# Kernel tuning notes

Hardware: AMD Instinct MI355X
Metric: run time of the kernel (lower is better)

Reference implementation:

```python
import jax, jax.numpy as jnp
import numpy as np

N_NODES = 50000
N_EDGES = 800000
D_IN, D_HID, D_OUT = 16, 64, 16
N_BLOCKS = 4


def setup_inputs() -> dict:
    key = jax.random.key(0)
    ks = jax.random.split(key, 12)
    s = 0.05  # small init scale to keep sum-aggregation over 4 blocks stable
    return {
        "x": jax.random.normal(ks[0], (N_NODES, D_IN), jnp.float32),
        "lframes": jax.random.normal(ks[1], (N_NODES, 4, 4), jnp.float32),
        "edge_index": jax.random.randint(ks[2], (2, N_EDGES), 0, N_NODES, jnp.int64),
        "lin_in_w": jax.random.normal(ks[3], (D_IN, D_HID), jnp.float32) * s,
        "lin_in_b": jnp.zeros((D_HID,), jnp.float32),
        # per-block mlp1: Linear(2D->D), ReLU, Linear(D->D), ReLU, Linear(D->D)
        "w0": jax.random.normal(ks[4], (N_BLOCKS, 2 * D_HID, D_HID), jnp.float32) * s,
        "b0": jnp.zeros((N_BLOCKS, D_HID), jnp.float32),
        "w1": jax.random.normal(ks[5], (N_BLOCKS, D_HID, D_HID), jnp.float32) * s,
        "b1": jnp.zeros((N_BLOCKS, D_HID), jnp.float32),
        "w2": jax.random.normal(ks[6], (N_BLOCKS, D_HID, D_HID), jnp.float32) * s,
        "b2": jnp.zeros((N_BLOCKS, D_HID), jnp.float32),
        "lin_out_w": jax.random.normal(ks[7], (D_HID, D_OUT), jnp.float32) * s,
        "lin_out_b": jnp.zeros((D_OUT,), jnp.float32),
    }


def reference(x, lframes, edge_index, lin_in_w, lin_in_b,
              w0, b0, w1, b1, w2, b2, lin_out_w, lin_out_b):
    src = edge_index[0]  # x_j (source / neighbor)
    dst = edge_index[1]  # x_i (target / aggregation node)
    h = x @ lin_in_w + lin_in_b  # [N, D]
    for k in range(N_BLOCKS):
        # message: cat((x_j, x_i)) -> mlp1 ; mlp2 is Identity (num_layers_mlp2=0)
        m = jnp.concatenate((h[src], h[dst]), axis=-1)  # [E, 2D]
        m = jax.nn.relu(m @ w0[k] + b0[k])
        m = jax.nn.relu(m @ w1[k] + b1[k])
        m = m @ w2[k] + b2[k]  # [E, D]
        # aggregate: scatter-add at target node
        h = jax.ops.segment_sum(m, dst, num_segments=N_NODES)
    return h @ lin_out_w + lin_out_b  # [N, D_OUT]
```

## Files before the change

### kernel.cpp

```cpp
#include <hip/hip_runtime.h>
#include <hip/hip_bf16.h>

#define N_NODES 50000
#define N_EDGES 800000
#define D_IN    16
#define D_HID   64
#define D_OUT   16
#define NCHUNK  ((N_NODES + 255) / 256)
#define TMAX    100352
#define GE8     ((N_EDGES / 8 + 255) / 256)
#define GH      ((N_NODES * D_HID + 255) / 256)
#define SCAP    48
#define NB      98
#define BCAP    12288

typedef __hip_bfloat16 bf16;
typedef _Float16 f16;
typedef _Float16 f16x8 __attribute__((ext_vector_type(8)));
typedef _Float16 f16x4 __attribute__((ext_vector_type(4)));
typedef float    f32x4 __attribute__((ext_vector_type(4)));
typedef _Float16 f16x8a __attribute__((ext_vector_type(8), may_alias));
typedef _Float16 f16x4a __attribute__((ext_vector_type(4), may_alias));
typedef unsigned short u16x8a __attribute__((ext_vector_type(8), may_alias));
typedef float    f32x4a __attribute__((ext_vector_type(4), may_alias));

__device__ __forceinline__ float b2f(bf16 v) { return __bfloat162float(v); }
__device__ __forceinline__ float bfb(unsigned short u) {
    union { unsigned u; float f; } z; z.u = (unsigned)u << 16; return z.f;
}
__device__ __forceinline__ int clampn(int v) {
    return v < 0 ? 0 : (v >= N_NODES ? N_NODES - 1 : v);
}
__device__ __forceinline__ float rdf(const void* p, long i, int isbf) {
    return isbf ? b2f(((const bf16*)p)[i]) : ((const float*)p)[i];
}
__device__ __forceinline__ f16x8 relu8(f16x8 v) {
#pragma unroll
    for (int j = 0; j < 8; j++) v[j] = v[j] > (f16)0 ? v[j] : (f16)0;
    return v;
}
__device__ __forceinline__ f16x4 relu4(f16x4 v) {
#pragma unroll
    for (int j = 0; j < 4; j++) v[j] = v[j] > (f16)0 ? v[j] : (f16)0;
    return v;
}
__device__ __forceinline__ int sbase(int m) {
    return (m & 0xFFFFF) * SCAP + ((m >> 25) & 3) * 16;
}

__global__ __launch_bounds__(256) void k_detect(const unsigned short* __restrict__ xw,
                                                const int* __restrict__ ei,
                                                int* __restrict__ flags,
                                                int* __restrict__ gbcnt,
                                                unsigned short* __restrict__ psrc_us)
{
    const int t = threadIdx.x;
    if (t < 64) psrc_us[(size_t)N_NODES * 64 + t] = 0xFC00u;
    if (t < NB) gbcnt[t] = 0;
    if (t == 0) {
        int inband = 0;
        for (int j = 0; j < 256; j++) {
            unsigned short w = xw[2 * j];
            int e = (w >> 7) & 0xFF;
            if ((w & 0x7FFF) == 0 || (e >= 100 && e <= 140)) inband++;
        }
        flags[0] = (inband >= 192) ? 1 : 0;
        int z = 1;
        for (int j = 1; j < 128; j += 2) z &= (ei[j] == 0) ? 1 : 0;
        flags[1] = z;
    }
}

__global__ __launch_bounds__(256) void k_prep(const int* __restrict__ flags,
                                              const void* __restrict__ gw0,
                                              const void* __restrict__ gw1,
                                              const void* __restrict__ gw2,
                                              f16* __restrict__ wfrag,
                                              const int* __restrict__ eidx,
                                              int* __restrict__ gbcnt,
                                              unsigned int* __restrict__ gbuckets,
                                              const void* __restrict__ x,
                                              const void* __restrict__ liw,
                                              const void* __restrict__ lib,
                                              float* __restrict__ h,
                                              const void* __restrict__ gb1,
                                              const void* __restrict__ gb2,
                                              float* __restrict__ cpad)
{
    const int isbf = flags[0];
    const int bid = blockIdx.x;
    if (bid < 32) {
        int idx = bid * 256 + threadIdx.x;
        int kb = idx >> 11, rem = idx & 2047;
        int slot = rem >> 6, lane = rem & 63;
        int lm = lane & 15, quad = lane >> 4;
        f16* outp = wfrag + (long)idx * 8;
        if (slot < 16) {
            int c = slot >> 2, q = slot & 3;
            long base = (long)kb * 2 * D_HID * D_HID;
#pragma unroll
            for (int j = 0; j < 8; j++)
                outp[j] = (f16)rdf(gw0, base + (long)(c * 32 + quad * 8 + j) * 64 + q * 16 + lm, isbf);
        } else {
            const void* gw = (slot < 24) ? gw1 : gw2;
            int s = (slot < 24) ? slot - 16 : slot - 24;
            int c = s >> 2, q = s & 3;
            long base = (long)kb * D_HID * D_HID;
#pragma unroll
            for (int j = 0; j < 8; j++)
                outp[j] = (f16)rdf(gw, base + (long)(c * 32 + quad * 8 + j) * 64 + q * 16 + lm, isbf);
        }
    } else if (bid < 32 + GE8) {
        __shared__ int cnt[NB], base[NB];
        const int t = threadIdx.x;
        for (int k = t; k < NB; k += 256) cnt[k] = 0;
        __syncthreads();
        const int ebase = ((bid - 32) * 256 + t) * 8;
        const int cntv = (ebase < N_EDGES) ? min(8, N_EDGES - ebase) : 0;
        const int strd = flags[1] ? 2 : 1;
        const long dbase = flags[1] ? (long)(2 * N_EDGES) : (long)N_EDGES;
        int d[8], s[8], r[8];
#pragma unroll
        for (int j = 0; j < 8; j++)
            if (j < cntv) {
                d[j] = clampn(eidx[dbase + (long)(ebase + j) * strd]);
                s[j] = clampn(eidx[(long)(ebase + j) * strd]);
            }
#pragma unroll
        for (int j = 0; j < 8; j++)
            if (j < cntv) r[j] = atomicAdd(&cnt[d[j] >> 9], 1);
        __syncthreads();
        for (int k = t; k < NB; k += 256)
            base[k] = cnt[k] ? atomicAdd(&gbcnt[k], cnt[k]) : 0;
        __syncthreads();
#pragma unroll
        for (int j = 0; j < 8; j++)
            if (j < cntv) {
                int b = d[j] >> 9;
                int p = base[b] + r[j];
                if (p < BCAP)
                    gbuckets[(size_t)b * BCAP + p] =
                        ((unsigned)(d[j] & 511) << 16) | (unsigned)s[j];
            }
    } else if (bid < 32 + GE8 + GH) {
        int idx = (bid - 32 - GE8) * 256 + threadIdx.x;
        if (idx >= N_NODES * D_HID) return;
        int n = idx >> 6, c = idx & 63;
        float acc, wr[16], xr[16];
        if (isbf) {
            const unsigned short* xp = (const unsigned short*)x + (long)n * 16;
            u16x8a x0 = *(const u16x8a*)xp, x1 = *(const u16x8a*)(xp + 8);
#pragma unroll
            for (int i = 0; i < 8; i++) { xr[i] = bfb(x0[i]); xr[8 + i] = bfb(x1[i]); }
            const unsigned short* wq = (const unsigned short*)liw;
#pragma unroll
            for (int i = 0; i < 16; i++) wr[i] = bfb(wq[i * 64 + c]);
            acc = bfb(((const unsigned short*)lib)[c]);
        } else {
            const float* xp = (const float*)x + (long)n * 16;
#pragma unroll
            for (int q = 0; q < 4; q++) {
                f32x4a v = *(const f32x4a*)(xp + q * 4);
#pragma unroll
                for (int j = 0; j < 4; j++) xr[q * 4 + j] = v[j];
            }
            const float* wq = (const float*)liw;
#pragma unroll
            for (int i = 0; i < 16; i++) wr[i] = wq[i * 64 + c];
            acc = ((const float*)lib)[c];
        }
#pragma unroll
        for (int i = 0; i < 16; i++) acc += xr[i] * wr[i];
        h[idx] = acc;
    } else {
        int t = threadIdx.x;
        int k = t >> 6, j = t & 63;
        float acc = rdf(gb2, (long)k * 64 + j, isbf);
        for (int i = 0; i < 64; i++) {
            float zi = (float)(f16)fmaxf(rdf(gb1, (long)k * 64 + i, isbf), 0.f);
            float wi = (float)(f16)rdf(gw2, (long)k * 4096 + (long)i * 64 + j, isbf);
            acc += zi * wi;
        }
        cpad[k * 64 + j] = acc;
    }
}

__global__ __launch_bounds__(256) void k_bucket(const int* __restrict__ gbcnt,
                                                const unsigned int* __restrict__ gbuckets,
                                                unsigned short* __restrict__ slots,
                                                int* __restrict__ deg,
                                                int* __restrict__ bsum_t)
{
    __shared__ unsigned short sl[512 * SCAP];
    __shared__ int cur[512];
    __shared__ int red[256];
    const int t = threadIdx.x, b = blockIdx.x;

    for (int k = t; k < 512; k += 256) cur[k] = 0;
    unsigned int* sl32 = (unsigned int*)sl;
    for (int k = t; k < 512 * SCAP / 2; k += 256) sl32[k] = 0xC350C350u;
    __syncthreads();

    const int ne = min(gbcnt[b], BCAP);
    const unsigned int* eb = gbuckets + (size_t)b * BCAP;
    for (int k = t; k < ne; k += 256) {
        unsigned int rec = eb[k];
        int n = rec >> 16;
        int pos = atomicAdd(&cur[n], 1);
        if (pos < SCAP) sl[n * SCAP + pos] = (unsigned short)(rec & 0xFFFFu);
    }
    __syncthreads();

    const int n0 = b * 512;
    const int nn = min(512, N_NODES - n0);
    unsigned int* gs32 = (unsigned int*)slots;
    for (int k = t; k < nn * SCAP / 2; k += 256)
        gs32[(size_t)n0 * SCAP / 2 + k] = sl32[k];
    for (int half = 0; half < 2; half++) {
        int n = half * 256 + t;
        int dv = (n < nn) ? cur[n] : 0;
        if (n < nn) deg[n0 + n] = dv;
        red[t] = min((dv + 15) >> 4, 3);
        __syncthreads();
        for (int d2 = 128; d2 > 0; d2 >>= 1) {
            if (t < d2) red[t] += red[t + d2];
            __syncthreads();
        }
        if (t == 0) bsum_t[b * 2 + half] = red[0];
        __syncthreads();
    }
}

__global__ __launch_bounds__(256) void k_scan2(const int* __restrict__ bsum_t,
                                               int* __restrict__ boff_t,
                                               int* __restrict__ tot_t)
{
    __shared__ int st_[256];
    const int t = threadIdx.x;
    st_[t] = (t < NCHUNK) ? bsum_t[t] : 0;
    __syncthreads();
    for (int d = 1; d < 256; d <<= 1) {
        int vt = (t >= d) ? st_[t - d] : 0;
        __syncthreads();
        st_[t] += vt;
        __syncthreads();
    }
    if (t < NCHUNK) boff_t[t] = (t == 0) ? 0 : st_[t - 1];
    if (t == NCHUNK - 1) tot_t[0] = st_[t];
}

__global__ __launch_bounds__(256) void k_scan3(const int* __restrict__ deg,
                                               const int* __restrict__ boff_t,
                                               int* __restrict__ toff,
                                               int* __restrict__ tmeta)
{
    __shared__ int st_[256];
    const int t = threadIdx.x;
    int i = blockIdx.x * 256 + t;
    int v = (i < N_NODES) ? deg[i] : 0;
    int w = min((v + 15) >> 4, 3);
    st_[t] = w;
    __syncthreads();
    for (int d = 1; d < 256; d <<= 1) {
        int ut = (t >= d) ? st_[t - d] : 0;
        __syncthreads();
        st_[t] += ut;
        __syncthreads();
    }
    if (i < N_NODES) {
        int exT = boff_t[blockIdx.x] + st_[t] - w;
        toff[i] = exT;
        for (int j = 0; j < w; j++)
            tmeta[exT + j] = i | (min(16, v - 16 * j) << 20) | (j << 25);
    }
}

#define HP_ST 72

__global__ __launch_bounds__(256) void k_proj(
    const int* __restrict__ flags, float* hio,
    const f16* __restrict__ wfrag, const void* __restrict__ gb0,
    const int* __restrict__ deg,
    f16* __restrict__ psrc, f16* __restrict__ pdst, int kblk)
{
    __shared__ f16 hL_s[4][16 * HP_ST];

    const int tid  = threadIdx.x;
    const int isbf = flags[0];
    const int wv = tid >> 6, ln = tid & 63;
    const int lm = ln & 15, quad = ln >> 4;
    f16* hL = hL_s[wv];

    const int g = blockIdx.x * 4 + wv;
    if (g >= N_NODES / 16) return;
    const int n0 = g * 16;

    const f16* wb = wfrag + (long)kblk * 32 * 64 * 8;

#pragma unroll
    for (int i = 0; i < 16; i++) {
        int idx = i * 64 + ln;
        hL[(idx >> 6) * HP_ST + (idx & 63)] = (f16)hio[(long)n0 * 64 + idx];
    }
#pragma unroll
    for (int i = 0; i < 16; i++)
        if (deg[n0 + i] == 0) hio[(long)(n0 + i) * 64 + ln] = 0.f;

    f16x8 a[2];
#pragma unroll
    for (int c = 0; c < 2; c++)
        a[c] = *(const f16x8a*)&hL[lm * HP_ST + c * 32 + quad * 8];

    f32x4 accS[4], accD[4];
#pragma unroll
    for (int q = 0; q < 4; q++) {
        float bd = rdf(gb0, (long)kblk * 64 + q * 16 + lm, isbf);
        accS[q] = (f32x4){0.f, 0.f, 0.f, 0.f};
        accD[q] = (f32x4){bd, bd, bd, bd};
    }
#pragma unroll
    for (int c = 0; c < 2; c++)
#pragma unroll
        for (int q = 0; q < 4; q++) {
            f16x8 bs = *(const f16x8a*)&wb[(((c + 0) * 4 + q) * 64 + ln) * 8];
            f16x8 bd = *(const f16x8a*)&wb[(((c + 2) * 4 + q) * 64 + ln) * 8];
            accS[q] = __builtin_amdgcn_mfma_f32_16x16x32_f16(a[c], bs, accS[q], 0, 0, 0);
            accD[q] = __builtin_amdgcn_mfma_f32_16x16x32_f16(a[c], bd, accD[q], 0, 0, 0);
        }
#pragma unroll
    for (int q = 0; q < 4; q++)
#pragma unroll
        for (int r = 0; r < 4; r++) {
            long o = (long)(n0 + quad * 4 + r) * 64 + q * 16 + lm;
            psrc[o] = (f16)accS[q][r];
            pdst[o] = (f16)accD[q][r];
        }
}

#define Y_ST 72

__global__ __launch_bounds__(256) void k_edge_tile(
    const int* __restrict__ flags,
    const unsigned short* __restrict__ slots, const int* __restrict__ tmeta,
    const int* __restrict__ toff,
    const f16* __restrict__ psrc, const f16* __restrict__ pdst,
    float* __restrict__ hout,
    const f16* __restrict__ wfrag, const void* __restrict__ gb1,
    const void* __restrict__ gb2, const float* __restrict__ cpad, int kblk)
{
    __shared__ f16 y_s[4][16 * Y_ST];
    __shared__ float b1L[64], b2L[64], cpL[64];

    const int tid  = threadIdx.x;
    const int isbf = flags[0];
    const int wv = tid >> 6, ln = tid & 63;
    const int lm = ln & 15, quad = ln >> 4;
    const int sub = ln & 7, eh = ln >> 3;
    f16* y = y_s[wv];

    if (tid < 64)       b1L[tid]       = rdf(gb1, (long)kblk * 64 + tid, isbf);
    else if (tid < 128) b2L[tid - 64]  = rdf(gb2, (long)kblk * 64 + (tid - 64), isbf);
    else if (tid < 192) cpL[tid - 128] = cpad[kblk * 64 + (tid - 128)];
    __syncthreads();

    const f16* wb = wfrag + (long)kblk * 32 * 64 * 8;
    f16x8 bw1[2][4], bw2[2][4];
#pragma unroll
    for (int c = 0; c < 2; c++)
#pragma unroll
        for (int q = 0; q < 4; q++) {
            bw1[c][q] = *(const f16x8a*)&wb[((16 + c * 4 + q) * 64 + ln) * 8];
            bw2[c][q] = *(const f16x8a*)&wb[((24 + c * 4 + q) * 64 + ln) * 8];
        }

    const int T  = toff[N_NODES];
    const int W  = gridDim.x * 4;
    const int gw = blockIdx.x * 4 + wv;
    int t0 = (int)((long)gw * T / W);
    int t1 = (int)((long)(gw + 1) * T / W);
    if (t0 > 0)
        while (t0 < T && (tmeta[t0] & 0xFFFFF) == (tmeta[t0 - 1] & 0xFFFFF)) t0++;
    if (t1 > 0)
        while (t1 < T && (tmeta[t1] & 0xFFFFF) == (tmeta[t1 - 1] & 0xFFFFF)) t1++;
    if (t0 >= t1) return;

    int mA = tmeta[t0];
    int mB = tmeta[min(t0 + 1, T - 1)];
    int mC = tmeta[min(t0 + 2, T - 1)];
    int bA = sbase(mA), bB = sbase(mB);
    int sAa = slots[bA + eh], sAb = slots[bA + 8 + eh];
    int sBa = slots[bB + eh], sBb = slots[bB + 8 + eh];
    f16x8 psAa = *(const f16x8a*)&psrc[(long)sAa * 64 + sub * 8];
    f16x8 psAb = *(const f16x8a*)&psrc[(long)sAb * 64 + sub * 8];
    f16x8 pdA  = *(const f16x8a*)&pdst[(long)(mA & 0xFFFFF) * 64 + sub * 8];

    f32x4 accv[4];
#pragma unroll
    for (int q = 0; q < 4; q++) accv[q] = (f32x4){0.f, 0.f, 0.f, 0.f};

    for (int tt = t0; tt < t1; ++tt) {
        const int mD = tmeta[min(tt + 3, T - 1)];
        const int bC = sbase(mC);
        const int sCa = slots[bC + eh], sCb = slots[bC + 8 + eh];
        f16x8 psBa = *(const f16x8a*)&psrc[(long)sBa * 64 + sub * 8];
        f16x8 psBb = *(const f16x8a*)&psrc[(long)sBb * 64 + sub * 8];
        f16x8 pdB  = *(const f16x8a*)&pdst[(long)(mB & 0xFFFFF) * 64 + sub * 8];

        *(f16x8a*)&y[eh * Y_ST + sub * 8]       = relu8(psAa + pdA);
        *(f16x8a*)&y[(8 + eh) * Y_ST + sub * 8] = relu8(psAb + pdA);

        f16x8 a1[2];
        a1[0] = *(const f16x8a*)&y[lm * Y_ST + quad * 8];
        a1[1] = *(const f16x8a*)&y[lm * Y_ST + 32 + quad * 8];
        f32x4 acc1[4];
#pragma unroll
        for (int q = 0; q < 4; q++)
            acc1[q] = *(const f32x4a*)&b1L[q * 16 + quad * 4];
#pragma unroll
        for (int c = 0; c < 2; c++)
#pragma unroll
            for (int q = 0; q < 4; q++)
                acc1[q] = __builtin_amdgcn_mfma_f32_16x16x32_f16(bw1[c][q], a1[c], acc1[q], 0, 0, 0);
#pragma unroll
        for (int q = 0; q < 4; q++) {
            f16x4 pk = { (f16)acc1[q][0], (f16)acc1[q][1],
                         (f16)acc1[q][2], (f16)acc1[q][3] };
            *(f16x4a*)&y[lm * Y_ST + q * 16 + quad * 4] = relu4(pk);
        }

        f16x8 a2[2];
        a2[0] = *(const f16x8a*)&y[lm * Y_ST + quad * 8];
        a2[1] = *(const f16x8a*)&y[lm * Y_ST + 32 + quad * 8];
#pragma unroll
        for (int c = 0; c < 2; c++)
#pragma unroll
            for (int q = 0; q < 4; q++)
                accv[q] = __builtin_amdgcn_mfma_f32_16x16x32_f16(a2[c], bw2[c][q], accv[q], 0, 0, 0);

        const int curn = mA & 0xFFFFF;
        const int nxt  = (tt + 1 < t1) ? (mB & 0xFFFFF) : -1;
        if (nxt != curn) {
            const float npad = (float)(16 - ((mA >> 20) & 31));
            const float nt16 = (float)((((mA >> 25) & 3) + 1) * 16);
#pragma unroll
            for (int q = 0; q < 4; q++) {
                float v = accv[q][0] + accv[q][1] + accv[q][2] + accv[q][3];
                v += __shfl_xor(v, 16, 64);
                v += __shfl_xor(v, 32, 64);
                if (quad == 0) {
                    const int f = q * 16 + lm;
                    hout[(long)curn * 64 + f] = v + nt16 * b2L[f] - npad * cpL[f];
                }
                accv[q] = (f32x4){0.f, 0.f, 0.f, 0.f};
            }
        }

        mA = mB; mB = mC; mC = mD;
        sBa = sCa; sBb = sCb;
        psAa = psBa; psAb = psBb; pdA = pdB;
    }
}

__global__ __launch_bounds__(256) void k_lin_out(const int* __restrict__ flags,
                                                 const float* __restrict__ h,
                                                 const void* __restrict__ w,
                                                 const void* __restrict__ b,
                                                 float* __restrict__ out)
{
    __shared__ float wl[D_HID * D_OUT];
    __shared__ float bl[D_OUT];
    const int isbf = flags[0];
    const int t = threadIdx.x;
    for (int k = t; k < D_HID * D_OUT; k += 256) wl[k] = rdf(w, k, isbf);
    if (t < D_OUT) bl[t] = rdf(b, t, isbf);
    __syncthreads();

    int idx = blockIdx.x * 256 + t;
    if (idx >= N_NODES * D_OUT) return;
    int n = idx >> 4, c = idx & 15;
    const float* hr = h + (long)n * D_HID;
    float acc = bl[c];
#pragma unroll
    for (int i = 0; i < 16; i++) {
        f32x4a v = *(const f32x4a*)(hr + i * 4);
        acc += v[0] * wl[(i * 4 + 0) * 16 + c] + v[1] * wl[(i * 4 + 1) * 16 + c]
             + v[2] * wl[(i * 4 + 2) * 16 + c] + v[3] * wl[(i * 4 + 3) * 16 + c];
    }
    out[idx] = acc;
}

extern "C" void kernel_launch(void* const* d_in, const int* in_sizes, int n_in,
                              void* d_out, int out_size, void* d_ws, size_t ws_size,
                              hipStream_t stream)
{
    const void* x    = d_in[0];
    const int*  ei   = (const int*)d_in[2];
    const void* liw  = d_in[3];
    const void* lib  = d_in[4];
    const void* w0   = d_in[5];
    const void* b0   = d_in[6];
    const void* w1   = d_in[7];
    const void* b1   = d_in[8];
    const void* w2   = d_in[9];
    const void* b2   = d_in[10];
    const void* low  = d_in[11];
    const void* lob  = d_in[12];
    float* out = (float*)d_out;

    char* wp = (char*)d_ws;
    int*   flags  = (int*)wp;                 wp += 256;
    float* hA     = (float*)wp;               wp += (size_t)N_NODES * D_HID * 4;
    f16*   Psrc   = (f16*)wp;                 wp += ((size_t)N_NODES + 1) * D_HID * 2;
    f16*   Pdst   = (f16*)wp;                 wp += (size_t)N_NODES * D_HID * 2;
    f16*   wfrag  = (f16*)wp;                 wp += (size_t)4 * 32 * 64 * 8 * 2;
    float* cpad   = (float*)wp;               wp += (size_t)4 * 64 * 4;
    int*   cursor = (int*)wp;                 wp += (size_t)N_NODES * 4;
    int*   bsum_t = (int*)wp;                 wp += 256 * 4;
    int*   boff_t = (int*)wp;                 wp += 256 * 4;
    int*   tmeta  = (int*)wp;                 wp += (size_t)TMAX * 4;
    unsigned short* slots = (unsigned short*)wp; wp += (size_t)N_NODES * SCAP * 2;
    int*   toff   = (int*)wp;                 wp += ((size_t)N_NODES + 4) * 4;
    int*   gbcnt  = (int*)wp;                 wp += 128 * 4;
    unsigned int* gbuckets = (unsigned int*)wp;

    k_detect<<<1, 256, 0, stream>>>((const unsigned short*)x, ei, flags,
                                    gbcnt, (unsigned short*)Psrc);
    k_prep<<<32 + GE8 + GH + 1, 256, 0, stream>>>(flags, w0, w1, w2, wfrag,
                                                  ei, gbcnt, gbuckets,
                                                  x, liw, lib, hA, b1, b2, cpad);
    k_bucket<<<NB, 256, 0, stream>>>(gbcnt, gbuckets, slots, cursor, bsum_t);

    k_scan2<<<1, 256, 0, stream>>>(bsum_t, boff_t, toff + N_NODES);
    k_scan3<<<NCHUNK, 256, 0, stream>>>(cursor, boff_t, toff, tmeta);

    for (int k = 0; k < 4; k++) {
        k_proj<<<(N_NODES / 16 + 3) / 4, 256, 0, stream>>>(flags, hA, wfrag, b0,
                                                           cursor, Psrc, Pdst, k);
        k_edge_tile<<<2048, 256, 0, stream>>>(flags, slots, tmeta, toff,
                                              Psrc, Pdst, hA, wfrag, b1, b2,
                                              cpad, k);
    }

    k_lin_out<<<(N_NODES * D_OUT + 255) / 256, 256, 0, stream>>>(flags, hA, low, lob, out);
}
```

Baseline: 396.2 us.

## Software-pipeline second MFMA layer across tiles with double-buffered LDS

Double-buffers the per-wave LDS activation tile so the second-layer MFMA and segment flush for the previous tile run in the next iteration, interleaved with the gathers and first-layer MFMA of the current tile. The goal is to break the serial dependency chain within each tile (LDS write, read, MFMA, write, read, MFMA) so MFMA and LDS latencies overlap. In exchange it doubles LDS per wave, raises register pressure by keeping a2 live, and adds an epilogue flush after the loop.

```diff
diff --git a/kernel.cpp b/kernel.cpp
--- a/kernel.cpp
+++ b/kernel.cpp
@@ -348,7 +348,7 @@
     const f16* __restrict__ wfrag, const void* __restrict__ gb1,
     const void* __restrict__ gb2, const float* __restrict__ cpad, int kblk)
 {
-    __shared__ f16 y_s[4][16 * Y_ST];
+    __shared__ f16 y_s[4][2][16 * Y_ST];
     __shared__ float b1L[64], b2L[64], cpL[64];
 
     const int tid  = threadIdx.x;
@@ -356,7 +356,6 @@
     const int wv = tid >> 6, ln = tid & 63;
     const int lm = ln & 15, quad = ln >> 4;
     const int sub = ln & 7, eh = ln >> 3;
-    f16* y = y_s[wv];
 
     if (tid < 64)       b1L[tid]       = rdf(gb1, (long)kblk * 64 + tid, isbf);
     else if (tid < 128) b2L[tid - 64]  = rdf(gb2, (long)kblk * 64 + (tid - 64), isbf);
@@ -384,9 +383,13 @@
         while (t1 < T && (tmeta[t1] & 0xFFFFF) == (tmeta[t1 - 1] & 0xFFFFF)) t1++;
     if (t0 >= t1) return;
 
+    f16* yW = y_s[wv][0];
+    f16* yR = y_s[wv][1];
+
     int mA = tmeta[t0];
     int mB = tmeta[min(t0 + 1, T - 1)];
     int mC = tmeta[min(t0 + 2, T - 1)];
+    int mP = 0;
     int bA = sbase(mA), bB = sbase(mB);
     int sAa = slots[bA + eh], sAb = slots[bA + 8 + eh];
     int sBa = slots[bB + eh], sBb = slots[bB + 8 + eh];
@@ -399,6 +402,13 @@
     for (int q = 0; q < 4; q++) accv[q] = (f32x4){0.f, 0.f, 0.f, 0.f};
 
     for (int tt = t0; tt < t1; ++tt) {
+        const bool hasP = (tt > t0);
+        f16x8 a2[2];
+        if (hasP) {
+            a2[0] = *(const f16x8a*)&yR[lm * Y_ST + quad * 8];
+            a2[1] = *(const f16x8a*)&yR[lm * Y_ST + 32 + quad * 8];
+        }
+
         const int mD = tmeta[min(tt + 3, T - 1)];
         const int bC = sbase(mC);
         const int sCa = slots[bC + eh], sCb = slots[bC + 8 + eh];
@@ -406,12 +416,12 @@
         f16x8 psBb = *(const f16x8a*)&psrc[(long)sBb * 64 + sub * 8];
         f16x8 pdB  = *(const f16x8a*)&pdst[(long)(mB & 0xFFFFF) * 64 + sub * 8];
 
-        *(f16x8a*)&y[eh * Y_ST + sub * 8]       = relu8(psAa + pdA);
-        *(f16x8a*)&y[(8 + eh) * Y_ST + sub * 8] = relu8(psAb + pdA);
+        *(f16x8a*)&yW[eh * Y_ST + sub * 8]       = relu8(psAa + pdA);
+        *(f16x8a*)&yW[(8 + eh) * Y_ST + sub * 8] = relu8(psAb + pdA);
 
         f16x8 a1[2];
-        a1[0] = *(const f16x8a*)&y[lm * Y_ST + quad * 8];
-        a1[1] = *(const f16x8a*)&y[lm * Y_ST + 32 + quad * 8];
+        a1[0] = *(const f16x8a*)&yW[lm * Y_ST + quad * 8];
+        a1[1] = *(const f16x8a*)&yW[lm * Y_ST + 32 + quad * 8];
         f32x4 acc1[4];
 #pragma unroll
         for (int q = 0; q < 4; q++)
@@ -425,39 +435,62 @@
         for (int q = 0; q < 4; q++) {
             f16x4 pk = { (f16)acc1[q][0], (f16)acc1[q][1],
                          (f16)acc1[q][2], (f16)acc1[q][3] };
-            *(f16x4a*)&y[lm * Y_ST + q * 16 + quad * 4] = relu4(pk);
-        }
-
+            *(f16x4a*)&yW[lm * Y_ST + q * 16 + quad * 4] = relu4(pk);
+        }
+
+        if (hasP) {
+#pragma unroll
+            for (int c = 0; c < 2; c++)
+#pragma unroll
+                for (int q = 0; q < 4; q++)
+                    accv[q] = __builtin_amdgcn_mfma_f32_16x16x32_f16(a2[c], bw2[c][q], accv[q], 0, 0, 0);
+            const int curn = mP & 0xFFFFF;
+            const int nxt  = mA & 0xFFFFF;
+            if (nxt != curn) {
+                const float npad = (float)(16 - ((mP >> 20) & 31));
+                const float nt16 = (float)((((mP >> 25) & 3) + 1) * 16);
+#pragma unroll
+                for (int q = 0; q < 4; q++) {
+                    float v = accv[q][0] + accv[q][1] + accv[q][2] + accv[q][3];
+                    v += __shfl_xor(v, 16, 64);
+                    v += __shfl_xor(v, 32, 64);
+                    if (quad == 0) {
+                        const int f = q * 16 + lm;
+                        hout[(long)curn * 64 + f] = v + nt16 * b2L[f] - npad * cpL[f];
+                    }
+                    accv[q] = (f32x4){0.f, 0.f, 0.f, 0.f};
+                }
+            }
+        }
+
+        mP = mA; mA = mB; mB = mC; mC = mD;
+        sBa = sCa; sBb = sCb;
+        psAa = psBa; psAb = psBb; pdA = pdB;
+        f16* ytmp = yW; yW = yR; yR = ytmp;
+    }
+
+    {
         f16x8 a2[2];
-        a2[0] = *(const f16x8a*)&y[lm * Y_ST + quad * 8];
-        a2[1] = *(const f16x8a*)&y[lm * Y_ST + 32 + quad * 8];
+        a2[0] = *(const f16x8a*)&yR[lm * Y_ST + quad * 8];
+        a2[1] = *(const f16x8a*)&yR[lm * Y_ST + 32 + quad * 8];
 #pragma unroll
         for (int c = 0; c < 2; c++)
 #pragma unroll
             for (int q = 0; q < 4; q++)
                 accv[q] = __builtin_amdgcn_mfma_f32_16x16x32_f16(a2[c], bw2[c][q], accv[q], 0, 0, 0);
-
-        const int curn = mA & 0xFFFFF;
-        const int nxt  = (tt + 1 < t1) ? (mB & 0xFFFFF) : -1;
-        if (nxt != curn) {
-            const float npad = (float)(16 - ((mA >> 20) & 31));
-            const float nt16 = (float)((((mA >> 25) & 3) + 1) * 16);
-#pragma unroll
-            for (int q = 0; q < 4; q++) {
-                float v = accv[q][0] + accv[q][1] + accv[q][2] + accv[q][3];
-                v += __shfl_xor(v, 16, 64);
-                v += __shfl_xor(v, 32, 64);
-                if (quad == 0) {
-                    const int f = q * 16 + lm;
-                    hout[(long)curn * 64 + f] = v + nt16 * b2L[f] - npad * cpL[f];
-                }
-                accv[q] = (f32x4){0.f, 0.f, 0.f, 0.f};
+        const int curn = mP & 0xFFFFF;
+        const float npad = (float)(16 - ((mP >> 20) & 31));
+        const float nt16 = (float)((((mP >> 25) & 3) + 1) * 16);
+#pragma unroll
+        for (int q = 0; q < 4; q++) {
+            float v = accv[q][0] + accv[q][1] + accv[q][2] + accv[q][3];
+            v += __shfl_xor(v, 16, 64);
+            v += __shfl_xor(v, 32, 64);
+            if (quad == 0) {
+                const int f = q * 16 + lm;
+                hout[(long)curn * 64 + f] = v + nt16 * b2L[f] - npad * cpL[f];
             }
         }
-
-        mA = mB; mB = mC; mC = mD;
-        sBa = sCa; sBb = sCb;
-        psAa = psBa; psAb = psBb; pdA = pdB;
     }
 }
 
```

Result: slower. 428.8 us (+8.2%).
